# Kernel optimization log

Measured on AMD Instinct MI355X. Metric: run time of the kernel, lower is better.

The kernel has to match this reference:

```python
import jax, jax.numpy as jnp
import numpy as np

B, D = 16384, 512
EPS_COS = 1e-8  # torch cosine_similarity eps


def setup_inputs() -> dict:
    key = jax.random.key(0)
    ks = jax.random.split(key, 8)
    rep1 = jax.random.normal(ks[0], (B, D), jnp.float32)
    rep2 = jax.random.normal(ks[1], (B, D), jnp.float32)
    rep3 = jax.random.normal(ks[2], (B, D), jnp.float32)
    hazard = jax.random.normal(ks[3], (B, 1), jnp.float32)
    # F.nll_loss expects log-probabilities
    score = jax.nn.log_softmax(jax.random.normal(ks[4], (B, 2), jnp.float32), axis=-1)
    time = jax.random.uniform(ks[5], (B,), jnp.float32)
    event = jax.random.randint(ks[6], (B,), 0, 2, dtype=jnp.int32)
    perm = jax.random.permutation(ks[7], B)  # deterministic stand-in for shuffle()
    x1_idx = perm[: B // 2].astype(jnp.int32)
    x2_idx = perm[B // 2 :].astype(jnp.int32)
    return dict(rep1=rep1, rep2=rep2, rep3=rep3, hazard=hazard, score=score,
                time=time, event=event, x1_idx=x1_idx, x2_idx=x2_idx)


def _normalize(r):
    n = jnp.maximum(jnp.linalg.norm(r, axis=-1, keepdims=True), EPS_COS)
    return r / n


def reference(rep1, rep2, rep3, hazard, score, time, event, x1_idx, x2_idx):
    trade_off, margin, alpha, beta = 0.3, 0.2, 0.5, 0.5
    ev_f = event.astype(score.dtype)

    # ---- cross-entropy term: F.nll_loss(log_probs, event) ----
    nll = -jnp.mean(jnp.take_along_axis(score, event[:, None].astype(jnp.int32), axis=1))

    # ---- Cox negative log-likelihood ----
    order = jnp.argsort(-time)            # descending time
    risk = hazard[order, 0]               # [B]
    evs = ev_f[order]
    log_risk = jnp.log(jnp.cumsum(jnp.exp(risk)) + 1e-6)
    cox = -jnp.sum((risk - log_risk) * evs) / (jnp.sum(evs) + 1e-6)

    # ---- contrastive loss (3 modalities, vectorized over pairs) ----
    R = jnp.stack([_normalize(rep1), _normalize(rep2), _normalize(rep3)])  # [M,B,D]
    x = R[:, x1_idx]  # [M,P,D]
    y = R[:, x2_idx]  # [M,P,D]
    pairs = [(0, 1), (0, 2), (1, 2)]
    dis_xx = sum((x[i] * x[j]).sum(-1) for i, j in pairs)  # [P]
    dis_yy = sum((y[i] * y[j]).sum(-1) for i, j in pairs)  # [P]
    dis_xy = (x * y).sum(-1).sum(0)                         # [P]
    con = jnp.mean(jnp.log1p(jnp.exp(margin + dis_xy - alpha * dis_xx - beta * dis_yy)))

    return nll + cox + trade_off * con
```

## Files before the change

### kernel.cpp

```cpp
#include <hip/hip_runtime.h>
#include <math.h>

#define B_N     16384
#define D_N     512
#define NPAIR   8192
#define NBUCKET 16384
#define CON_BLOCKS 2048
#define STAT_BLOCKS 64
#define BIG_BLOCKS (CON_BLOCKS + STAT_BLOCKS)
#define COX_BLOCKS 64
#define POISON_U   0xAAAAAAAAu

__device__ __forceinline__ float wave_reduce(float v) {
    #pragma unroll
    for (int m = 32; m >= 1; m >>= 1) v += __shfl_xor(v, m, 64);
    return v;
}

__device__ __forceinline__ float dot4(float4 a, float4 b) {
    return a.x*b.x + a.y*b.y + a.z*b.z + a.w*b.w;
}

__device__ __forceinline__ int bucket_of(float t) {
    return min(max((int)(t * 16384.0f), 0), NBUCKET - 1);
}

__device__ __forceinline__ unsigned long long key_of(float t, int i) {
    return (((unsigned long long)__float_as_uint(t)) << 14) |
           (unsigned long long)(B_N - 1 - i);
}

__global__ __launch_bounds__(256) void k_big(
        const float* __restrict__ rep1,
        const float* __restrict__ rep2,
        const float* __restrict__ rep3,
        const float* __restrict__ hazard,
        const float* __restrict__ score,
        const float* __restrict__ time,
        const int*   __restrict__ event,
        const int*   __restrict__ x1_idx,
        const int*   __restrict__ x2_idx,
        float* __restrict__ partCon,
        float* __restrict__ partNll,
        float* __restrict__ partEv,
        float* __restrict__ sumE,
        int*   __restrict__ head,
        int*   __restrict__ next)
{
    __shared__ float sh0[4], sh1[4];
    const int tid  = threadIdx.x;
    const int lane = tid & 63;
    const int wave = tid >> 6;

    if (blockIdx.x < CON_BLOCKS) {
        const int p  = blockIdx.x * 4 + wave;
        const int ia = x1_idx[p];
        const int ib = x2_idx[p];
        const float4* A1 = (const float4*)(rep1 + (size_t)ia * D_N);
        const float4* A2 = (const float4*)(rep2 + (size_t)ia * D_N);
        const float4* A3 = (const float4*)(rep3 + (size_t)ia * D_N);
        const float4* B1 = (const float4*)(rep1 + (size_t)ib * D_N);
        const float4* B2 = (const float4*)(rep2 + (size_t)ib * D_N);
        const float4* B3 = (const float4*)(rep3 + (size_t)ib * D_N);

        float v[15];
        #pragma unroll
        for (int k = 0; k < 15; ++k) v[k] = 0.f;
        #pragma unroll
        for (int r = 0; r < 2; ++r) {
            const int k = lane + r * 64;
            float4 a1 = A1[k], a2 = A2[k], a3 = A3[k];
            float4 b1 = B1[k], b2 = B2[k], b3 = B3[k];
            v[0]  += dot4(a1, a1); v[1]  += dot4(a2, a2); v[2]  += dot4(a3, a3);
            v[3]  += dot4(b1, b1); v[4]  += dot4(b2, b2); v[5]  += dot4(b3, b3);
            v[6]  += dot4(a1, a2); v[7]  += dot4(a1, a3); v[8]  += dot4(a2, a3);
            v[9]  += dot4(b1, b2); v[10] += dot4(b1, b3); v[11] += dot4(b2, b3);
            v[12] += dot4(a1, b1); v[13] += dot4(a2, b2); v[14] += dot4(a3, b3);
        }
        #pragma unroll
        for (int k = 0; k < 15; ++k) v[k] = wave_reduce(v[k]);

        if (lane == 0) {
            float n1a = fmaxf(sqrtf(v[0]), 1e-8f), n2a = fmaxf(sqrtf(v[1]), 1e-8f), n3a = fmaxf(sqrtf(v[2]), 1e-8f);
            float n1b = fmaxf(sqrtf(v[3]), 1e-8f), n2b = fmaxf(sqrtf(v[4]), 1e-8f), n3b = fmaxf(sqrtf(v[5]), 1e-8f);
            float dxx = v[6]/(n1a*n2a) + v[7]/(n1a*n3a) + v[8]/(n2a*n3a);
            float dyy = v[9]/(n1b*n2b) + v[10]/(n1b*n3b) + v[11]/(n2b*n3b);
            float dxy = v[12]/(n1a*n1b) + v[13]/(n2a*n2b) + v[14]/(n3a*n3b);
            float s = 0.2f + dxy - 0.5f*dxx - 0.5f*dyy;
            sh0[wave] = log1pf(expf(s));
        }
        __syncthreads();
        if (tid == 0)
            partCon[blockIdx.x] = sh0[0] + sh0[1] + sh0[2] + sh0[3];
    } else {
        const int sb = blockIdx.x - CON_BLOCKS;
        const int i  = sb * 256 + tid;
        const float t = time[i];
        const float e = __expf(hazard[i]);
        const int   b = bucket_of(t);
        atomicAdd(&sumE[b], e);
        const int old = atomicExch(&head[b], i + 1);
        next[i] = old;

        const int ev = event[i];
        float nll_p = wave_reduce(score[i * 2 + ev]);
        float ev_p  = wave_reduce((float)ev);
        if (lane == 0) { sh0[wave] = nll_p; sh1[wave] = ev_p; }
        __syncthreads();
        if (tid == 0) {
            partNll[sb] = sh0[0] + sh0[1] + sh0[2] + sh0[3];
            partEv[sb]  = sh1[0] + sh1[1] + sh1[2] + sh1[3];
        }
    }
}

__global__ __launch_bounds__(1024) void k_scan(const float* __restrict__ sumE,
                                               float* __restrict__ cumH)
{
    __shared__ float lsf[1024];
    const int tid = threadIdx.x;
    const int base = tid * 16;

    float f[16]; float fs = 0.f;
    #pragma unroll
    for (int k = 0; k < 16; ++k) { f[k] = sumE[base + k]; fs += f[k]; }
    lsf[tid] = fs;
    __syncthreads();
    for (int d = 1; d < 1024; d <<= 1) {
        float v = (tid >= d) ? lsf[tid - d] : 0.f;
        __syncthreads();
        lsf[tid] += v;
        __syncthreads();
    }
    const float total = lsf[1023];
    float running = total - lsf[tid];
    #pragma unroll
    for (int k = 15; k >= 0; --k) { cumH[base + k] = running; running += f[k]; }
}

__global__ __launch_bounds__(256) void k_cox(
        const float* __restrict__ hazard,
        const float* __restrict__ time,
        const int*   __restrict__ event,
        const int*   __restrict__ head,
        const int*   __restrict__ next,
        const float* __restrict__ cumH,
        const float* __restrict__ partCon,
        const float* __restrict__ partNll,
        const float* __restrict__ partEv,
        float* __restrict__ partCox,
        unsigned* __restrict__ doneCox,
        float* __restrict__ out)
{
    __shared__ float shX[4];
    __shared__ int lastflag;
    const int tid  = threadIdx.x;
    const int lane = tid & 63;
    const int wave = tid >> 6;
    const int i = blockIdx.x * 256 + tid;

    const float t = time[i];
    const float h = hazard[i];
    const int   b = bucket_of(t);
    const unsigned long long ki = key_of(t, i);

    float cum = cumH[b] + __expf(h);
    int p = head[b];
    while (p >= 1 && p <= B_N) {
        const int j = p - 1;
        const float tj = time[j];
        if (key_of(tj, j) > ki) cum += __expf(hazard[j]);
        p = next[j];
    }
    float cox_p = event[i] ? (h - logf(cum + 1e-6f)) : 0.f;
    cox_p = wave_reduce(cox_p);
    if (lane == 0) shX[wave] = cox_p;
    __syncthreads();
    if (tid == 0)
        atomicExch(&partCox[blockIdx.x], shX[0] + shX[1] + shX[2] + shX[3]);

    __threadfence();
    if (tid == 0)
        lastflag = (atomicAdd(doneCox, 1u) == POISON_U + (COX_BLOCKS - 1));
    __syncthreads();
    if (lastflag) {
        float con = 0.f;
        #pragma unroll
        for (int k = 0; k < CON_BLOCKS / 256; ++k) con += partCon[tid + k * 256];
        float cox = 0.f, nll = 0.f, ev = 0.f;
        if (tid < COX_BLOCKS) {
            cox = atomicAdd(&partCox[tid], 0.f);
            nll = partNll[tid];
            ev  = partEv[tid];
        }
        con = wave_reduce(con);
        cox = wave_reduce(cox);
        nll = wave_reduce(nll);
        ev  = wave_reduce(ev);
        __syncthreads();
        if (lane == 0) { shX[wave] = con; }
        __syncthreads();
        float C = shX[0] + shX[1] + shX[2] + shX[3];
        if (lane == 0) { shX[wave] = cox; }
        __syncthreads();
        float X = shX[0] + shX[1] + shX[2] + shX[3];
        if (lane == 0) { shX[wave] = nll; }
        __syncthreads();
        float N = shX[0] + shX[1] + shX[2] + shX[3];
        if (lane == 0) { shX[wave] = ev; }
        __syncthreads();
        float E = shX[0] + shX[1] + shX[2] + shX[3];
        if (tid == 0)
            out[0] = (-N / (float)B_N) + (-X / (E + 1e-6f)) + 0.3f * (C / (float)NPAIR);
    }
}

extern "C" void kernel_launch(void* const* d_in, const int* in_sizes, int n_in,
                              void* d_out, int out_size, void* d_ws, size_t ws_size,
                              hipStream_t stream)
{
    const float* rep1   = (const float*)d_in[0];
    const float* rep2   = (const float*)d_in[1];
    const float* rep3   = (const float*)d_in[2];
    const float* hazard = (const float*)d_in[3];
    const float* score  = (const float*)d_in[4];
    const float* time_  = (const float*)d_in[5];
    const int*   event  = (const int*)d_in[6];
    const int*   x1     = (const int*)d_in[7];
    const int*   x2     = (const int*)d_in[8];
    float* out = (float*)d_out;

    char* w = (char*)d_ws;
    float*    sumE    = (float*)   (w + 0);
    int*      head    = (int*)     (w + 65536);
    unsigned* doneCox = (unsigned*)(w + 131072);
    int*      next    = (int*)     (w + 131136);
    float*    cumH    = (float*)   (w + 196672);
    float*    partCon = (float*)   (w + 262208);
    float*    partNll = (float*)   (w + 270400);
    float*    partEv  = (float*)   (w + 270656);
    float*    partCox = (float*)   (w + 270912);

    k_big  <<<BIG_BLOCKS, 256, 0, stream>>>(rep1, rep2, rep3, hazard, score, time_,
                                            event, x1, x2, partCon, partNll, partEv,
                                            sumE, head, next);
    k_scan <<<1, 1024, 0, stream>>>(sumE, cumH);
    k_cox  <<<COX_BLOCKS, 256, 0, stream>>>(hazard, time_, event, head, next, cumH,
                                            partCon, partNll, partEv, partCox,
                                            doneCox, out);
}
```

Measured before the change: 148.4 us.

## Fuse bucket prefix scan into Cox kernel and halve bucket count

```diff
diff --git a/kernel.cpp b/kernel.cpp
--- a/kernel.cpp
+++ b/kernel.cpp
@@ -4,7 +4,7 @@
 #define B_N     16384
 #define D_N     512
 #define NPAIR   8192
-#define NBUCKET 16384
+#define NBUCKET 8192
 #define CON_BLOCKS 2048
 #define STAT_BLOCKS 64
 #define BIG_BLOCKS (CON_BLOCKS + STAT_BLOCKS)
@@ -22,7 +22,7 @@
 }
 
 __device__ __forceinline__ int bucket_of(float t) {
-    return min(max((int)(t * 16384.0f), 0), NBUCKET - 1);
+    return min(max((int)(t * 8192.0f), 0), NBUCKET - 1);
 }
 
 __device__ __forceinline__ unsigned long long key_of(float t, int i) {
@@ -114,37 +114,13 @@
     }
 }
 
-__global__ __launch_bounds__(1024) void k_scan(const float* __restrict__ sumE,
-                                               float* __restrict__ cumH)
-{
-    __shared__ float lsf[1024];
-    const int tid = threadIdx.x;
-    const int base = tid * 16;
-
-    float f[16]; float fs = 0.f;
-    #pragma unroll
-    for (int k = 0; k < 16; ++k) { f[k] = sumE[base + k]; fs += f[k]; }
-    lsf[tid] = fs;
-    __syncthreads();
-    for (int d = 1; d < 1024; d <<= 1) {
-        float v = (tid >= d) ? lsf[tid - d] : 0.f;
-        __syncthreads();
-        lsf[tid] += v;
-        __syncthreads();
-    }
-    const float total = lsf[1023];
-    float running = total - lsf[tid];
-    #pragma unroll
-    for (int k = 15; k >= 0; --k) { cumH[base + k] = running; running += f[k]; }
-}
-
 __global__ __launch_bounds__(256) void k_cox(
         const float* __restrict__ hazard,
         const float* __restrict__ time,
         const int*   __restrict__ event,
         const int*   __restrict__ head,
         const int*   __restrict__ next,
-        const float* __restrict__ cumH,
+        const float* __restrict__ sumE,
         const float* __restrict__ partCon,
         const float* __restrict__ partNll,
         const float* __restrict__ partEv,
@@ -152,19 +128,42 @@
         unsigned* __restrict__ doneCox,
         float* __restrict__ out)
 {
+    __shared__ float cumL[NBUCKET];
+    __shared__ float psum[256];
     __shared__ float shX[4];
     __shared__ int lastflag;
     const int tid  = threadIdx.x;
     const int lane = tid & 63;
     const int wave = tid >> 6;
+
+    const int base = tid * 32;
+    float fs = 0.f;
+    #pragma unroll
+    for (int k = 0; k < 32; ++k) fs += sumE[base + k];
+    psum[tid] = fs;
+    __syncthreads();
+    for (int d = 1; d < 256; d <<= 1) {
+        float v = (tid >= d) ? psum[tid - d] : 0.f;
+        __syncthreads();
+        psum[tid] += v;
+        __syncthreads();
+    }
+    const float total = psum[255];
+    float run = total - psum[tid];
+    #pragma unroll
+    for (int k = 31; k >= 0; --k) {
+        cumL[k * 256 + tid] = run;
+        run += sumE[base + k];
+    }
+    __syncthreads();
+
     const int i = blockIdx.x * 256 + tid;
-
     const float t = time[i];
     const float h = hazard[i];
     const int   b = bucket_of(t);
     const unsigned long long ki = key_of(t, i);
 
-    float cum = cumH[b] + __expf(h);
+    float cum = cumL[(b & 31) * 256 + (b >> 5)] + __expf(h);
     int p = head[b];
     while (p >= 1 && p <= B_N) {
         const int j = p - 1;
@@ -232,20 +231,18 @@
 
     char* w = (char*)d_ws;
     float*    sumE    = (float*)   (w + 0);
-    int*      head    = (int*)     (w + 65536);
-    unsigned* doneCox = (unsigned*)(w + 131072);
-    int*      next    = (int*)     (w + 131136);
-    float*    cumH    = (float*)   (w + 196672);
-    float*    partCon = (float*)   (w + 262208);
-    float*    partNll = (float*)   (w + 270400);
-    float*    partEv  = (float*)   (w + 270656);
-    float*    partCox = (float*)   (w + 270912);
-
-    k_big  <<<BIG_BLOCKS, 256, 0, stream>>>(rep1, rep2, rep3, hazard, score, time_,
-                                            event, x1, x2, partCon, partNll, partEv,
-                                            sumE, head, next);
-    k_scan <<<1, 1024, 0, stream>>>(sumE, cumH);
-    k_cox  <<<COX_BLOCKS, 256, 0, stream>>>(hazard, time_, event, head, next, cumH,
-                                            partCon, partNll, partEv, partCox,
-                                            doneCox, out);
-}
+    int*      head    = (int*)     (w + 32768);
+    unsigned* doneCox = (unsigned*)(w + 65536);
+    int*      next    = (int*)     (w + 65600);
+    float*    partCon = (float*)   (w + 131136);
+    float*    partNll = (float*)   (w + 139328);
+    float*    partEv  = (float*)   (w + 139584);
+    float*    partCox = (float*)   (w + 139840);
+
+    k_big <<<BIG_BLOCKS, 256, 0, stream>>>(rep1, rep2, rep3, hazard, score, time_,
+                                           event, x1, x2, partCon, partNll, partEv,
+                                           sumE, head, next);
+    k_cox <<<COX_BLOCKS, 256, 0, stream>>>(hazard, time_, event, head, next, sumE,
+                                           partCon, partNll, partEv, partCox,
+                                           doneCox, out);
+}
```

New measurement: 145.2 us. 2.2% less time.
